# Kernel optimization log

Hardware: AMD Instinct MI355X
Metric: run time of the kernel (lower is better)

The kernel has to match this reference:

```python
import jax, jax.numpy as jnp
import numpy as np

H = 5  # hidden size of both LSTMs

def _lstm_layer(x, Wih, Whh, bih, bhh):
    """x: [B,T,I] -> hs: [B,T,H]. PyTorch gate order i,f,g,o; zero init state."""
    B, T, _ = x.shape
    # precompute input contribution for all timesteps: [T,B,4H]
    xg = (jnp.einsum('bti,gi->btg', x, Wih) + bih + bhh).transpose(1, 0, 2)
    def step(carry, xg_t):
        h, c = carry
        g = xg_t + h @ Whh.T
        i, f, gg, o = jnp.split(g, 4, axis=-1)
        c = jax.nn.sigmoid(f) * c + jax.nn.sigmoid(i) * jnp.tanh(gg)
        h = jax.nn.sigmoid(o) * jnp.tanh(c)
        return (h, c), h
    h0 = jnp.zeros((B, H), x.dtype)
    (_, _), hs = jax.lax.scan(step, (h0, h0), xg)
    return hs.transpose(1, 0, 2)  # [B,T,H]

def setup_inputs() -> dict:
    key = jax.random.key(0)
    ks = jax.random.split(key, 32)
    B, T = 16384, 128
    def u(k, shape, fan):
        s = 1.0 / np.sqrt(fan)
        return jax.random.uniform(k, shape, jnp.float32, -s, s)
    inp = {
        'x1': jax.random.normal(ks[0], (B, T, 5), jnp.float32),
        'x2': jax.random.normal(ks[1], (B, T, 5), jnp.float32),
        # lstm1 (1 layer)
        'Wih1': u(ks[2], (4*H, 5), H), 'Whh1': u(ks[3], (4*H, H), H),
        'bih1': u(ks[4], (4*H,), H), 'bhh1': u(ks[5], (4*H,), H),
        # lstm2 layer 0
        'Wih2a': u(ks[6], (4*H, 5), H), 'Whh2a': u(ks[7], (4*H, H), H),
        'bih2a': u(ks[8], (4*H,), H), 'bhh2a': u(ks[9], (4*H,), H),
        # lstm2 layer 1
        'Wih2b': u(ks[10], (4*H, H), H), 'Whh2b': u(ks[11], (4*H, H), H),
        'bih2b': u(ks[12], (4*H,), H), 'bhh2b': u(ks[13], (4*H,), H),
        # FC stack 20->32->32->16->16->5
        'W1': u(ks[14], (32, 20), 20), 'b1': u(ks[15], (32,), 20),
        'W2': u(ks[16], (32, 32), 32), 'b2': u(ks[17], (32,), 32),
        'W3': u(ks[18], (16, 32), 32), 'b3': u(ks[19], (16,), 32),
        'W4': u(ks[20], (16, 16), 16), 'b4': u(ks[21], (16,), 16),
        'W5': u(ks[22], (5, 16), 16), 'b5': u(ks[23], (5,), 16),
    }
    return inp

def reference(x1, x2, Wih1, Whh1, bih1, bhh1, Wih2a, Whh2a, bih2a, bhh2a,
              Wih2b, Whh2b, bih2b, bhh2b, W1, b1, W2, b2, W3, b3, W4, b4, W5, b5):
    out1 = _lstm_layer(x1, Wih1, Whh1, bih1, bhh1)[:, -1, :]            # [B,5]
    h2 = _lstm_layer(x2, Wih2a, Whh2a, bih2a, bhh2a)                    # [B,T,5]
    out2 = _lstm_layer(h2, Wih2b, Whh2b, bih2b, bhh2b)[:, -1, :]        # [B,5]
    out = jnp.concatenate([x1[:, -1, :], x2[:, -1, :], out1, out2], axis=1)  # [B,20]
    out = jax.nn.relu(out @ W1.T + b1)
    out = jax.nn.relu(out @ W2.T + b2)
    out = jax.nn.relu(out @ W3.T + b3)
    out = jax.nn.relu(out @ W4.T + b4)
    return out @ W5.T + b5  # [B,5]
```

## Files before the change

kernel.cpp:

```cpp
#include <hip/hip_runtime.h>

#define DEV __device__ __forceinline__

DEV float fexp2(float x) { return __builtin_amdgcn_exp2f(x); }
DEV float frcp(float x) { return __builtin_amdgcn_rcpf(x); }

template <int S>
DEV float qbcast(float x) {
#if __has_builtin(__builtin_amdgcn_update_dpp)
  int i = __float_as_int(x);
  i = __builtin_amdgcn_update_dpp(0, i, S * 0x55, 0xF, 0xF, true);
  return __int_as_float(i);
#else
  return __shfl(x, S, 4);
#endif
}

struct Cell {
  float wih[5][5];
  float whh[5][5];
  float b[5];
};

DEV void load_cell(Cell& W, const float* __restrict__ Wih,
                   const float* __restrict__ Whh, const float* __restrict__ bih,
                   const float* __restrict__ bhh, int s) {
#pragma unroll
  for (int j = 0; j < 5; ++j) {
    int r = 5 * s + j;
#pragma unroll
    for (int k = 0; k < 5; ++k) {
      W.wih[j][k] = Wih[r * 5 + k];
      W.whh[j][k] = Whh[r * 5 + k];
    }
    W.b[j] = bih[r] + bhh[r];
  }
}

DEV void cell_step(const Cell& W, float kexp, float m2, float a2,
                   const float x[5], float h[5], float c[5]) {
  float a[5];
#pragma unroll
  for (int j = 0; j < 5; ++j) {
    float acc = W.b[j];
#pragma unroll
    for (int k = 0; k < 5; ++k) acc = fmaf(W.wih[j][k], x[k], acc);
#pragma unroll
    for (int k = 0; k < 5; ++k) acc = fmaf(W.whh[j][k], h[k], acc);
    float e = fexp2(acc * kexp);
    float r = frcp(1.0f + e);
    a[j] = fmaf(m2, r, a2);
  }
#pragma unroll
  for (int j = 0; j < 5; ++j) {
    float I = qbcast<0>(a[j]);
    float F = qbcast<1>(a[j]);
    float G = qbcast<2>(a[j]);
    float O = qbcast<3>(a[j]);
    float cj = fmaf(F, c[j], I * G);
    c[j] = cj;
    float e2 = fexp2(cj * -2.885390082f);
    float tc = fmaf(2.0f, frcp(1.0f + e2), -1.0f);
    h[j] = O * tc;
  }
}

DEV void lds_copy(float* dst, const float* __restrict__ src, int n, int tid) {
  for (int i = tid; i < n; i += 256) dst[i] = src[i];
}

__global__ __launch_bounds__(256, 1) void rnn_fused_kernel(
    const float* __restrict__ x1, const float* __restrict__ x2,
    const float* __restrict__ Wih1, const float* __restrict__ Whh1,
    const float* __restrict__ bih1, const float* __restrict__ bhh1,
    const float* __restrict__ Wih2a, const float* __restrict__ Whh2a,
    const float* __restrict__ bih2a, const float* __restrict__ bhh2a,
    const float* __restrict__ Wih2b, const float* __restrict__ Whh2b,
    const float* __restrict__ bih2b, const float* __restrict__ bhh2b,
    const float* __restrict__ W1, const float* __restrict__ b1,
    const float* __restrict__ W2, const float* __restrict__ b2,
    const float* __restrict__ W3, const float* __restrict__ b3,
    const float* __restrict__ W4, const float* __restrict__ b4,
    const float* __restrict__ W5, const float* __restrict__ b5,
    float* __restrict__ out, int B) {
  __shared__ __align__(16) float sFC[2613];
  {
    int tl = threadIdx.x;
    lds_copy(sFC + 0, W1, 640, tl);
    lds_copy(sFC + 640, b1, 32, tl);
    lds_copy(sFC + 672, W2, 1024, tl);
    lds_copy(sFC + 1696, b2, 32, tl);
    lds_copy(sFC + 1728, W3, 512, tl);
    lds_copy(sFC + 2240, b3, 16, tl);
    lds_copy(sFC + 2256, W4, 256, tl);
    lds_copy(sFC + 2512, b4, 16, tl);
    lds_copy(sFC + 2528, W5, 80, tl);
    lds_copy(sFC + 2608, b5, 5, tl);
  }
  __syncthreads();

  int tid = blockIdx.x * 256 + threadIdx.x;
  int e = tid >> 2;
  int s = tid & 3;
  if (e >= B) return;

  Cell WA, WB, WC;
  load_cell(WA, Wih1, Whh1, bih1, bhh1, s);
  load_cell(WB, Wih2a, Whh2a, bih2a, bhh2a, s);
  load_cell(WC, Wih2b, Whh2b, bih2b, bhh2b, s);

  const float kexp = (s == 2) ? -2.885390082f : -1.442695041f;
  const float m2 = (s == 2) ? 2.0f : 1.0f;
  const float a2 = (s == 2) ? -1.0f : 0.0f;

  const float* px1 = x1 + (size_t)e * 640;
  const float* px2 = x2 + (size_t)e * 640;

  float h1[5], c1[5], h2a[5], c2a[5], h2b[5], c2b[5];
#pragma unroll
  for (int k = 0; k < 5; ++k) {
    h1[k] = c1[k] = h2a[k] = c2a[k] = h2b[k] = c2b[k] = 0.0f;
  }

  float xa[5], xb[5];
#pragma unroll
  for (int k = 0; k < 5; ++k) {
    xa[k] = px1[k];
    xb[k] = px2[k];
  }

  for (int t = 0; t < 128; ++t) {
    int tn = (t < 127) ? t + 1 : 127;
    float nxa[5], nxb[5];
#pragma unroll
    for (int k = 0; k < 5; ++k) {
      nxa[k] = px1[tn * 5 + k];
      nxb[k] = px2[tn * 5 + k];
    }
    cell_step(WA, kexp, m2, a2, xa, h1, c1);
    cell_step(WB, kexp, m2, a2, xb, h2a, c2a);
    cell_step(WC, kexp, m2, a2, h2a, h2b, c2b);
#pragma unroll
    for (int k = 0; k < 5; ++k) {
      xa[k] = nxa[k];
      xb[k] = nxb[k];
    }
  }

  float in0[20];
#pragma unroll
  for (int k = 0; k < 5; ++k) {
    in0[k] = xa[k];
    in0[5 + k] = xb[k];
    in0[10 + k] = h1[k];
    in0[15 + k] = h2b[k];
  }
  float v1[32];
#pragma unroll
  for (int n = 0; n < 32; ++n) {
    float acc = sFC[640 + n];
#pragma unroll
    for (int k = 0; k < 20; ++k) acc = fmaf(sFC[n * 20 + k], in0[k], acc);
    v1[n] = fmaxf(acc, 0.0f);
  }
  float v2[32];
#pragma unroll
  for (int n = 0; n < 32; ++n) {
    float acc = sFC[1696 + n];
#pragma unroll
    for (int k = 0; k < 32; ++k) acc = fmaf(sFC[672 + n * 32 + k], v1[k], acc);
    v2[n] = fmaxf(acc, 0.0f);
  }
  float v3[16];
#pragma unroll
  for (int n = 0; n < 16; ++n) {
    float acc = sFC[2240 + n];
#pragma unroll
    for (int k = 0; k < 32; ++k) acc = fmaf(sFC[1728 + n * 32 + k], v2[k], acc);
    v3[n] = fmaxf(acc, 0.0f);
  }
  float v4[16];
#pragma unroll
  for (int n = 0; n < 16; ++n) {
    float acc = sFC[2512 + n];
#pragma unroll
    for (int k = 0; k < 16; ++k) acc = fmaf(sFC[2256 + n * 16 + k], v3[k], acc);
    v4[n] = fmaxf(acc, 0.0f);
  }
  if (s == 0) {
#pragma unroll
    for (int n = 0; n < 5; ++n) {
      float acc = sFC[2608 + n];
#pragma unroll
      for (int k = 0; k < 16; ++k)
        acc = fmaf(sFC[2528 + n * 16 + k], v4[k], acc);
      out[(size_t)e * 5 + n] = acc;
    }
  }
}

extern "C" void kernel_launch(void* const* d_in, const int* in_sizes, int n_in,
                              void* d_out, int out_size, void* d_ws,
                              size_t ws_size, hipStream_t stream) {
  const float* x1 = (const float*)d_in[0];
  const float* x2 = (const float*)d_in[1];
  const float* Wih1 = (const float*)d_in[2];
  const float* Whh1 = (const float*)d_in[3];
  const float* bih1 = (const float*)d_in[4];
  const float* bhh1 = (const float*)d_in[5];
  const float* Wih2a = (const float*)d_in[6];
  const float* Whh2a = (const float*)d_in[7];
  const float* bih2a = (const float*)d_in[8];
  const float* bhh2a = (const float*)d_in[9];
  const float* Wih2b = (const float*)d_in[10];
  const float* Whh2b = (const float*)d_in[11];
  const float* bih2b = (const float*)d_in[12];
  const float* bhh2b = (const float*)d_in[13];
  const float* W1 = (const float*)d_in[14];
  const float* b1 = (const float*)d_in[15];
  const float* W2 = (const float*)d_in[16];
  const float* b2 = (const float*)d_in[17];
  const float* W3 = (const float*)d_in[18];
  const float* b3 = (const float*)d_in[19];
  const float* W4 = (const float*)d_in[20];
  const float* b4 = (const float*)d_in[21];
  const float* W5 = (const float*)d_in[22];
  const float* b5 = (const float*)d_in[23];

  int B = in_sizes[0] / 640;
  int threads = B * 4;
  int blocks = (threads + 255) / 256;

  rnn_fused_kernel<<<blocks, 256, 0, stream>>>(
      x1, x2, Wih1, Whh1, bih1, bhh1, Wih2a, Whh2a, bih2a, bhh2a, Wih2b, Whh2b,
      bih2b, bhh2b, W1, b1, W2, b2, W3, b3, W4, b4, W5, b5, (float*)d_out, B);
}
```

Before: 253.1 us.

## Pipeline the three LSTM cells across lane quads with bpermute handoff

The work is split differently: each 64-lane wavefront now handles 5 batch elements, with a separate 4-lane quad for each of the three LSTM cells. The layer-2 cell runs one timestep behind and gets layer-1's hidden state from the neighbouring quad through ds_bpermute. This shortens each thread's serial dependency chain by a factor of three and cuts the register weights per thread to one cell. The FC stack now runs cooperatively across the wave through small shared buffers, with weights read directly from global memory. The costs are that 4 of 64 lanes sit idle, the bpermute adds latency on every step, and the FC stage adds barriers.

```diff
diff --git a/kernel.cpp b/kernel.cpp
--- a/kernel.cpp
+++ b/kernel.cpp
@@ -7,13 +7,14 @@
 
 template <int S>
 DEV float qbcast(float x) {
-#if __has_builtin(__builtin_amdgcn_update_dpp)
   int i = __float_as_int(x);
   i = __builtin_amdgcn_update_dpp(0, i, S * 0x55, 0xF, 0xF, true);
   return __int_as_float(i);
-#else
-  return __shfl(x, S, 4);
-#endif
+}
+
+DEV float bperm(int byte_addr, float x) {
+  return __int_as_float(
+      __builtin_amdgcn_ds_bpermute(byte_addr, __float_as_int(x)));
 }
 
 struct Cell {
@@ -65,11 +66,7 @@
   }
 }
 
-DEV void lds_copy(float* dst, const float* __restrict__ src, int n, int tid) {
-  for (int i = tid; i < n; i += 256) dst[i] = src[i];
-}
-
-__global__ __launch_bounds__(256, 1) void rnn_fused_kernel(
+__global__ __launch_bounds__(64, 4) void rnn_pipe_kernel(
     const float* __restrict__ x1, const float* __restrict__ x2,
     const float* __restrict__ Wih1, const float* __restrict__ Whh1,
     const float* __restrict__ bih1, const float* __restrict__ bhh1,
@@ -83,119 +80,128 @@
     const float* __restrict__ W4, const float* __restrict__ b4,
     const float* __restrict__ W5, const float* __restrict__ b5,
     float* __restrict__ out, int B) {
-  __shared__ __align__(16) float sFC[2613];
-  {
-    int tl = threadIdx.x;
-    lds_copy(sFC + 0, W1, 640, tl);
-    lds_copy(sFC + 640, b1, 32, tl);
-    lds_copy(sFC + 672, W2, 1024, tl);
-    lds_copy(sFC + 1696, b2, 32, tl);
-    lds_copy(sFC + 1728, W3, 512, tl);
-    lds_copy(sFC + 2240, b3, 16, tl);
-    lds_copy(sFC + 2256, W4, 256, tl);
-    lds_copy(sFC + 2512, b4, 16, tl);
-    lds_copy(sFC + 2528, W5, 80, tl);
-    lds_copy(sFC + 2608, b5, 5, tl);
-  }
-  __syncthreads();
-
-  int tid = blockIdx.x * 256 + threadIdx.x;
-  int e = tid >> 2;
-  int s = tid & 3;
-  if (e >= B) return;
-
-  Cell WA, WB, WC;
-  load_cell(WA, Wih1, Whh1, bih1, bhh1, s);
-  load_cell(WB, Wih2a, Whh2a, bih2a, bhh2a, s);
-  load_cell(WC, Wih2b, Whh2b, bih2b, bhh2b, s);
-
-  const float kexp = (s == 2) ? -2.885390082f : -1.442695041f;
-  const float m2 = (s == 2) ? 2.0f : 1.0f;
-  const float a2 = (s == 2) ? -1.0f : 0.0f;
-
-  const float* px1 = x1 + (size_t)e * 640;
-  const float* px2 = x2 + (size_t)e * 640;
-
-  float h1[5], c1[5], h2a[5], c2a[5], h2b[5], c2b[5];
-#pragma unroll
-  for (int k = 0; k < 5; ++k) {
-    h1[k] = c1[k] = h2a[k] = c2a[k] = h2b[k] = c2b[k] = 0.0f;
-  }
-
-  float xa[5], xb[5];
-#pragma unroll
-  for (int k = 0; k < 5; ++k) {
-    xa[k] = px1[k];
-    xb[k] = px2[k];
-  }
-
-  for (int t = 0; t < 128; ++t) {
-    int tn = (t < 127) ? t + 1 : 127;
-    float nxa[5], nxb[5];
+  __shared__ float sIn[5][20];
+  __shared__ float sA[5][32];
+  __shared__ float sB[5][32];
+
+  const int lane = threadIdx.x;
+  const int q = lane >> 2;
+  const int s = lane & 3;
+
+  if (q < 15) {
+    const int e_w = q / 3;
+    const int cell = q - e_w * 3;
+    const int eg = blockIdx.x * 5 + e_w;
+    const int egc = (eg < B) ? eg : (B - 1);
+    const bool c2 = (cell == 2);
+    const float* xbase = (cell == 1) ? x2 : x1;
+    const float* px = xbase + (size_t)egc * 640;
+
+    Cell W;
+    if (cell == 0)
+      load_cell(W, Wih1, Whh1, bih1, bhh1, s);
+    else if (cell == 1)
+      load_cell(W, Wih2a, Whh2a, bih2a, bhh2a, s);
+    else
+      load_cell(W, Wih2b, Whh2b, bih2b, bhh2b, s);
+
+    const float kexp = (s == 2) ? -2.885390082f : -1.442695041f;
+    const float m2 = (s == 2) ? 2.0f : 1.0f;
+    const float a2 = (s == 2) ? -1.0f : 0.0f;
+    const int bpaddr = ((c2 ? lane - 4 : lane) << 2);
+
+    float h[5], c[5], hp[5], xcur[5];
 #pragma unroll
     for (int k = 0; k < 5; ++k) {
-      nxa[k] = px1[tn * 5 + k];
-      nxb[k] = px2[tn * 5 + k];
-    }
-    cell_step(WA, kexp, m2, a2, xa, h1, c1);
-    cell_step(WB, kexp, m2, a2, xb, h2a, c2a);
-    cell_step(WC, kexp, m2, a2, h2a, h2b, c2b);
-#pragma unroll
-    for (int k = 0; k < 5; ++k) {
-      xa[k] = nxa[k];
-      xb[k] = nxb[k];
-    }
-  }
-
-  float in0[20];
-#pragma unroll
-  for (int k = 0; k < 5; ++k) {
-    in0[k] = xa[k];
-    in0[5 + k] = xb[k];
-    in0[10 + k] = h1[k];
-    in0[15 + k] = h2b[k];
-  }
-  float v1[32];
-#pragma unroll
-  for (int n = 0; n < 32; ++n) {
-    float acc = sFC[640 + n];
-#pragma unroll
-    for (int k = 0; k < 20; ++k) acc = fmaf(sFC[n * 20 + k], in0[k], acc);
-    v1[n] = fmaxf(acc, 0.0f);
-  }
-  float v2[32];
-#pragma unroll
-  for (int n = 0; n < 32; ++n) {
-    float acc = sFC[1696 + n];
-#pragma unroll
-    for (int k = 0; k < 32; ++k) acc = fmaf(sFC[672 + n * 32 + k], v1[k], acc);
-    v2[n] = fmaxf(acc, 0.0f);
-  }
-  float v3[16];
-#pragma unroll
-  for (int n = 0; n < 16; ++n) {
-    float acc = sFC[2240 + n];
-#pragma unroll
-    for (int k = 0; k < 32; ++k) acc = fmaf(sFC[1728 + n * 32 + k], v2[k], acc);
-    v3[n] = fmaxf(acc, 0.0f);
-  }
-  float v4[16];
-#pragma unroll
-  for (int n = 0; n < 16; ++n) {
-    float acc = sFC[2512 + n];
-#pragma unroll
-    for (int k = 0; k < 16; ++k) acc = fmaf(sFC[2256 + n * 16 + k], v3[k], acc);
-    v4[n] = fmaxf(acc, 0.0f);
-  }
-  if (s == 0) {
-#pragma unroll
-    for (int n = 0; n < 5; ++n) {
-      float acc = sFC[2608 + n];
-#pragma unroll
-      for (int k = 0; k < 16; ++k)
-        acc = fmaf(sFC[2528 + n * 16 + k], v4[k], acc);
-      out[(size_t)e * 5 + n] = acc;
-    }
+      h[k] = c[k] = hp[k] = 0.0f;
+      xcur[k] = px[k];
+    }
+
+    for (int t = 0; t < 128; ++t) {
+      const int tn = (t < 127) ? t + 1 : 127;
+      float xn[5];
+#pragma unroll
+      for (int k = 0; k < 5; ++k) xn[k] = px[tn * 5 + k];
+      float xin[5];
+#pragma unroll
+      for (int k = 0; k < 5; ++k) xin[k] = c2 ? hp[k] : xcur[k];
+      cell_step(W, kexp, m2, a2, xin, h, c);
+      if (t == 0 && c2) {
+#pragma unroll
+        for (int k = 0; k < 5; ++k) {
+          h[k] = 0.0f;
+          c[k] = 0.0f;
+        }
+      }
+#pragma unroll
+      for (int k = 0; k < 5; ++k) hp[k] = bperm(bpaddr, h[k]);
+#pragma unroll
+      for (int k = 0; k < 5; ++k) xcur[k] = xn[k];
+    }
+    if (c2) {
+      float xin[5];
+#pragma unroll
+      for (int k = 0; k < 5; ++k) xin[k] = hp[k];
+      cell_step(W, kexp, m2, a2, xin, h, c);
+    }
+
+    if (eg < B && s == 0) {
+      if (cell == 0) {
+#pragma unroll
+        for (int k = 0; k < 5; ++k) {
+          sIn[e_w][k] = xcur[k];
+          sIn[e_w][10 + k] = h[k];
+        }
+      } else if (cell == 1) {
+#pragma unroll
+        for (int k = 0; k < 5; ++k) sIn[e_w][5 + k] = xcur[k];
+      } else {
+#pragma unroll
+        for (int k = 0; k < 5; ++k) sIn[e_w][15 + k] = h[k];
+      }
+    }
+  }
+  __syncthreads();
+
+  for (int task = lane; task < 160; task += 64) {
+    int e = task >> 5, n = task & 31;
+    float acc = b1[n];
+#pragma unroll
+    for (int k = 0; k < 20; ++k) acc = fmaf(W1[n * 20 + k], sIn[e][k], acc);
+    sA[e][n] = fmaxf(acc, 0.0f);
+  }
+  __syncthreads();
+  for (int task = lane; task < 160; task += 64) {
+    int e = task >> 5, n = task & 31;
+    float acc = b2[n];
+#pragma unroll
+    for (int k = 0; k < 32; ++k) acc = fmaf(W2[n * 32 + k], sA[e][k], acc);
+    sB[e][n] = fmaxf(acc, 0.0f);
+  }
+  __syncthreads();
+  for (int task = lane; task < 80; task += 64) {
+    int e = task >> 4, n = task & 15;
+    float acc = b3[n];
+#pragma unroll
+    for (int k = 0; k < 32; ++k) acc = fmaf(W3[n * 32 + k], sB[e][k], acc);
+    sA[e][n] = fmaxf(acc, 0.0f);
+  }
+  __syncthreads();
+  for (int task = lane; task < 80; task += 64) {
+    int e = task >> 4, n = task & 15;
+    float acc = b4[n];
+#pragma unroll
+    for (int k = 0; k < 16; ++k) acc = fmaf(W4[n * 16 + k], sA[e][k], acc);
+    sB[e][n] = fmaxf(acc, 0.0f);
+  }
+  __syncthreads();
+  for (int task = lane; task < 25; task += 64) {
+    int e = task / 5, n = task - 5 * (task / 5);
+    float acc = b5[n];
+#pragma unroll
+    for (int k = 0; k < 16; ++k) acc = fmaf(W5[n * 16 + k], sB[e][k], acc);
+    int eg = blockIdx.x * 5 + e;
+    if (eg < B) out[(size_t)eg * 5 + n] = acc;
   }
 }
 
@@ -228,10 +234,9 @@
   const float* b5 = (const float*)d_in[23];
 
   int B = in_sizes[0] / 640;
-  int threads = B * 4;
-  int blocks = (threads + 255) / 256;
-
-  rnn_fused_kernel<<<blocks, 256, 0, stream>>>(
+  int blocks = (B + 4) / 5;
+
+  rnn_pipe_kernel<<<blocks, 64, 0, stream>>>(
       x1, x2, Wih1, Whh1, bih1, bhh1, Wih2a, Whh2a, bih2a, bhh2a, Wih2b, Whh2b,
       bih2b, bhh2b, W1, b1, W2, b2, W3, b3, W4, b4, W5, b5, (float*)d_out, B);
 }
```

Result: slower. 271.3 us (+7.2%).
